# Optimization experiments

Hardware: AMD Instinct MI355X
Metric: run time of the kernel (lower is better)

## Reference

```python
import jax, jax.numpy as jnp
import numpy as np

N, SD, VD, ED, E, NG, NA, NB = 512, 256, 128, 128, 262144, 16, 16, 5


def _lin_init(key, fan_in, fan_out):
    # torch.nn.Linear default: U(-1/sqrt(fan_in), 1/sqrt(fan_in)); stored as (in, out)
    lim = 1.0 / np.sqrt(fan_in)
    return jax.random.uniform(key, (fan_in, fan_out), jnp.float32, -lim, lim)


def setup_inputs() -> dict:
    key = jax.random.key(0)
    ks = jax.random.split(key, 20)
    s = jax.random.normal(ks[0], (N, SD), jnp.float32)
    v = jax.random.normal(ks[1], (N, 3, VD), jnp.float32)
    p = jax.random.normal(ks[2], (N, 3), jnp.float32)
    e = jax.random.normal(ks[3], (E, ED), jnp.float32)
    batch = jnp.sort(jax.random.randint(ks[4], (N,), 0, NG))
    edge_index_global = jax.random.randint(ks[5], (2, E), 0, N)
    W_sm = _lin_init(ks[6], SD, SD); b_sm = jnp.zeros((SD,), jnp.float32)
    W_bm = _lin_init(ks[7], ED, SD); b_bm = jnp.zeros((SD,), jnp.float32)
    W_b0 = _lin_init(ks[8], SD + 1, SD); b_b0 = jnp.zeros((SD,), jnp.float32)
    W_b1 = _lin_init(ks[9], SD, NB); b_b1 = jnp.zeros((NB,), jnp.float32)
    W_c = _lin_init(ks[10], VD, 1)  # no bias
    W_a = _lin_init(ks[11], SD, NA); b_a = jnp.zeros((NA,), jnp.float32)
    return {"s": s, "v": v, "p": p, "e": e, "batch": batch,
            "edge_index_global": edge_index_global,
            "W_sm": W_sm, "b_sm": b_sm, "W_bm": W_bm, "b_bm": b_bm,
            "W_b0": W_b0, "b_b0": b_b0, "W_b1": W_b1, "b_b1": b_b1,
            "W_c": W_c, "W_a": W_a, "b_a": b_a}


def reference(s, v, p, e, batch, edge_index_global,
              W_sm, b_sm, W_bm, b_bm, W_b0, b_b0, W_b1, b_b1, W_c, W_a, b_a):
    # shared_mapping: Linear + SiLU
    s = jax.nn.silu(s @ W_sm + b_sm)                      # [N, SD]
    coords_pred = (v @ W_c)[..., 0]                       # [N, 3]
    atoms_pred = s @ W_a + b_a                            # [N, NA]
    j, i = edge_index_global[0], edge_index_global[1]
    n = s.shape[0]
    # coords_param == 'data': coords = p + pred, then per-graph mean centering
    coords_pred = p + coords_pred
    seg_sum = jax.ops.segment_sum(coords_pred, batch, num_segments=NG)
    counts = jax.ops.segment_sum(jnp.ones((n, 1), coords_pred.dtype), batch, num_segments=NG)
    mean = seg_sum / jnp.maximum(counts, 1.0)
    coords_pred = coords_pred - mean[batch]
    # squared pairwise distance per edge
    d = jnp.sum((coords_pred[i] - coords_pred[j]) ** 2, axis=-1, keepdims=True)  # [E, 1]
    # sparse -> dense -> sparse symmetrization of edge features (as in the source)
    e_dense = jnp.zeros((n, n, e.shape[-1]), e.dtype).at[j, i].set(e)
    e_dense = 0.5 * (e_dense + jnp.transpose(e_dense, (1, 0, 2)))
    e_sym = e_dense[j, i]                                 # [E, ED]
    f = s[i] + s[j] + (e_sym @ W_bm + b_bm)               # [E, SD]
    edge = jnp.concatenate([f, d], axis=-1)               # [E, SD+1]
    bonds_pred = jax.nn.silu(edge @ W_b0 + b_b0) @ W_b1 + b_b1  # [E, NB]
    return coords_pred, atoms_pred, bonds_pred
```

## Files before the change

### kernel.cpp

```cpp
#include <hip/hip_runtime.h>
#include <math.h>

#define N_NODES 512
#define SD_ 256
#define VD_ 128
#define ED_ 128
#define NE_ 262144
#define NG_ 16
#define NA_ 16
#define NB_ 5
#define MAXP 131328

typedef __attribute__((ext_vector_type(8))) short bf16x8;
typedef __attribute__((ext_vector_type(4))) float f32x4;

__device__ __forceinline__ float silu_f(float x) { return x / (1.0f + expf(-x)); }
__device__ __forceinline__ float silu_fast(float x) {
    return x * __builtin_amdgcn_rcpf(1.0f + __builtin_amdgcn_exp2f(x * -1.44269504f));
}
__device__ __forceinline__ unsigned short f2bf(float x) {
    unsigned int u = __float_as_uint(x);
    return (unsigned short)((u + 0x7fffu + ((u >> 16) & 1u)) >> 16);
}
__device__ __forceinline__ float bf2f(unsigned short h) {
    return __uint_as_float(((unsigned int)h) << 16);
}
__device__ __forceinline__ unsigned int cvt_pk_bf16(float lo, float hi) {
    unsigned int r;
    asm("v_cvt_pk_bf16_f32 %0, %1, %2" : "=v"(r) : "v"(lo), "v"(hi));
    return r;
}

__global__ __launch_bounds__(256) void prep_a(
    const int* __restrict__ ei, int* __restrict__ emap,
    const float* __restrict__ W_bm, const float* __restrict__ W_b0,
    unsigned short* __restrict__ WfF,
    const float* __restrict__ s, const float* __restrict__ v, const float* __restrict__ p,
    const float* __restrict__ W_sm, const float* __restrict__ b_sm,
    const float* __restrict__ W_a, const float* __restrict__ b_a,
    const float* __restrict__ W_c,
    const float* __restrict__ b_bm, const float* __restrict__ b_b0,
    float* __restrict__ s2f, float* __restrict__ cpred, float* __restrict__ atoms_out,
    int* __restrict__ counter, float* __restrict__ zrow, float* __restrict__ bias2)
{
    __shared__ float srow[8][SD_];
    __shared__ float s2row[8][SD_];
    const int bid = blockIdx.x;
    const int tid = threadIdx.x;

    if (bid < 1024) {
        int k = bid * 256 + tid;
        int j = ei[k], i = ei[NE_ + k];
        atomicMax(&emap[j * N_NODES + i], k);
        return;
    }
    if (bid < 1040) {
        int mtg = bid - 1024;
        int kb = tid >> 6;
        int l  = tid & 63;
        int m  = mtg * 16 + (l & 15);
        int k0 = kb * 32 + (l >> 4) * 8;
        float a8[8];
        #pragma unroll
        for (int i = 0; i < 8; ++i) a8[i] = 0.f;
        for (int c = 0; c < SD_; ++c) {
            float wb0 = W_b0[(size_t)c * SD_ + m];
            #pragma unroll
            for (int i = 0; i < 8; ++i)
                a8[i] = fmaf(W_bm[(size_t)(k0 + i) * SD_ + c], wb0, a8[i]);
        }
        bf16x8 pack;
        #pragma unroll
        for (int i = 0; i < 8; ++i) pack[i] = (short)f2bf(a8[i]);
        int idx = (mtg * 4 + kb) * 64 + l;
        *(bf16x8*)(WfF + (size_t)idx * 8) = pack;
        return;
    }
    if (bid < 1104) {
        const int n0 = (bid - 1040) * 8;
        #pragma unroll
        for (int n = 0; n < 8; ++n) srow[n][tid] = s[(size_t)(n0 + n) * SD_ + tid];
        __syncthreads();
        float acc[8];
        {
            float bb = b_sm[tid];
            #pragma unroll
            for (int n = 0; n < 8; ++n) acc[n] = bb;
        }
        #pragma unroll 4
        for (int c = 0; c < SD_; ++c) {
            float wv = W_sm[(size_t)c * SD_ + tid];
            #pragma unroll
            for (int n = 0; n < 8; ++n) acc[n] = fmaf(srow[n][c], wv, acc[n]);
        }
        #pragma unroll
        for (int n = 0; n < 8; ++n) {
            float sv = silu_f(acc[n]);
            s2f[(size_t)(n0 + n) * SD_ + tid] = sv;
            s2row[n][tid] = sv;
        }
        __syncthreads();
        if (tid < 128) {
            int n = tid >> 4, a = tid & 15;
            float x = b_a[a];
            #pragma unroll 8
            for (int c = 0; c < SD_; ++c) x = fmaf(s2row[n][c], W_a[(size_t)c * NA_ + a], x);
            atoms_out[(size_t)(n0 + n) * NA_ + a] = x;
        }
        return;
    }
    if (bid == 1104) {
        if (tid == 0) counter[0] = 0;
        if (tid < ED_) zrow[tid] = 0.0f;
        for (int o = tid; o < N_NODES * 3; o += 256) {
            float x = p[o];
            const float* vr = v + (size_t)o * VD_;
            #pragma unroll 8
            for (int c = 0; c < VD_; ++c) x = fmaf(vr[c], W_c[c], x);
            cpred[o] = x;
        }
        return;
    }
    {
        float acc = b_b0[tid];
        for (int c = 0; c < SD_; ++c)
            acc = fmaf(b_bm[c], W_b0[(size_t)c * SD_ + tid], acc);
        bias2[tid] = acc;
    }
}

__global__ __launch_bounds__(512) void prep_b(
    const float* __restrict__ cpred, const int* __restrict__ batch,
    float* __restrict__ coords_ws, float* __restrict__ coords_out,
    const int* __restrict__ emap, int* __restrict__ counter,
    int* __restrict__ pairslot, int4* __restrict__ worklist,
    const float* __restrict__ s2f, const float* __restrict__ W_b0,
    float* __restrict__ S2W)
{
    __shared__ float cl[N_NODES * 3];
    __shared__ int   bl[N_NODES];
    __shared__ float meanv[NG_ * 3];
    const int tid = threadIdx.x;
    const int bid = blockIdx.x;

    if (bid == 0) {
        bl[tid] = batch[tid];
        #pragma unroll
        for (int dd = 0; dd < 3; ++dd) cl[tid * 3 + dd] = cpred[tid * 3 + dd];
        __syncthreads();
        if (tid < NG_ * 3) {
            int g = tid / 3, dd = tid % 3;
            float sum = 0.f; int cnt = 0;
            for (int n = 0; n < N_NODES; ++n) {
                if (bl[n] == g) { sum += cl[n * 3 + dd]; cnt++; }
            }
            meanv[tid] = sum / (float)(cnt > 0 ? cnt : 1);
        }
        __syncthreads();
        int g = bl[tid];
        #pragma unroll
        for (int dd = 0; dd < 3; ++dd) {
            float val = cl[tid * 3 + dd] - meanv[g * 3 + dd];
            coords_ws[tid * 3 + dd]  = val;
            coords_out[tid * 3 + dd] = val;
        }
        return;
    }
    if (bid <= 512) {
        int idx = (bid - 1) * 512 + tid;
        int a = idx >> 9, b = idx & (N_NODES - 1);
        bool lower = (a <= b);
        int k1 = -1, k2 = -1;
        if (lower) {
            k1 = emap[(a << 9) | b];
            k2 = emap[(b << 9) | a];
        }
        bool qual = lower && (k1 >= 0 || k2 >= 0);
        unsigned long long mask = __ballot(qual);
        if (mask == 0ull) return;
        int lane = tid & 63;
        int leader = __ffsll((unsigned long long)mask) - 1;
        int base = 0;
        if (lane == leader) base = atomicAdd(counter, __popcll(mask));
        base = __shfl(base, leader);
        if (qual) {
            int slot = base + __popcll(mask & ((1ull << lane) - 1ull));
            pairslot[(a << 9) | b] = slot;
            pairslot[(b << 9) | a] = slot;
            worklist[slot] = make_int4(a, b, k1, k2);
        }
        return;
    }
    {
        __shared__ float srows[2][SD_];
        int n0 = (bid - 513) * 2;
        if (tid < 512) {
            int n = tid >> 8, c = tid & 255;
            srows[n][c] = s2f[(size_t)(n0 + n) * SD_ + c];
        }
        __syncthreads();
        int n = tid >> 8, m = tid & 255;
        float acc = 0.f;
        #pragma unroll 8
        for (int c = 0; c < SD_; ++c)
            acc = fmaf(srows[n][c], W_b0[(size_t)c * SD_ + m], acc);
        S2W[(size_t)(n0 + n) * SD_ + m] = acc;
    }
}

__global__ __launch_bounds__(256) void bonds_scatter(
    const int* __restrict__ ei, const int* __restrict__ pairslot,
    const float* __restrict__ repval, float* __restrict__ bonds_out)
{
    int k = blockIdx.x * 256 + threadIdx.x;
    int j = ei[k], i = ei[NE_ + k];
    int slot = pairslot[(j << 9) | i];
    const float* rp = repval + (size_t)slot * NB_;
    #pragma unroll
    for (int b = 0; b < NB_; ++b)
        bonds_out[(size_t)k * NB_ + b] = rp[b];
}

__global__ __launch_bounds__(512) void edge_mfma(
    const float* __restrict__ e, const int4* __restrict__ worklist,
    const int* __restrict__ counter, const float* __restrict__ coords,
    const float* __restrict__ zrow,
    const unsigned short* __restrict__ WfF, const float* __restrict__ S2W,
    const float* __restrict__ bias2,
    const float* __restrict__ W_b1, const float* __restrict__ W_b0_last,
    const float* __restrict__ b_b1,
    float* __restrict__ repval)
{
    const int blk = blockIdx.x;
    const int cnt = counter[0];
    if (blk * 64 >= cnt) return;

    __shared__ __align__(16) unsigned short esym_lds[64 * 128];
    __shared__ unsigned short wb1t[NB_ * 256];
    __shared__ float bonds_part[8 * 64 * NB_];
    __shared__ float dw[64];
    __shared__ int li_s[64], lj_s[64];

    const int tid = threadIdx.x;
    const int l   = tid & 63;
    const int w   = tid >> 6;
    const int eLo = l & 15;
    const int hi  = l >> 4;

    bf16x8 a1pf[4][2];
    #pragma unroll
    for (int kb = 0; kb < 4; ++kb)
        #pragma unroll
        for (int mt = 0; mt < 2; ++mt)
            a1pf[kb][mt] = *(const bf16x8*)(WfF + ((size_t)(((w * 2 + mt) * 4 + kb) * 64 + l) * 8));

    if (tid < 256) {
        const int eL = l;
        const int q  = w;
        int widx = min(blk * 64 + eL, cnt - 1);
        int4 wk = worklist[widx];
        const float* r1 = (wk.z >= 0) ? (e + (size_t)wk.z * ED_) : zrow;
        const float* r2 = (wk.w >= 0) ? (e + (size_t)wk.w * ED_) : zrow;
        const float4* p1 = (const float4*)(r1 + q * 32);
        const float4* p2 = (const float4*)(r2 + q * 32);
        float4 va[8], vb[8];
        #pragma unroll
        for (int t = 0; t < 8; ++t) va[t] = p1[t];
        #pragma unroll
        for (int t = 0; t < 8; ++t) vb[t] = p2[t];
        #pragma unroll
        for (int t = 0; t < 8; ++t) {
            va[t].x += vb[t].x; va[t].y += vb[t].y;
            va[t].z += vb[t].z; va[t].w += vb[t].w;
        }
        int ntB = eL >> 4, eLoB = eL & 15;
        #pragma unroll
        for (int h2 = 0; h2 < 4; ++h2) {
            float4 x0 = va[h2 * 2], x1 = va[h2 * 2 + 1];
            uint4 c;
            c.x = cvt_pk_bf16(0.5f * x0.x, 0.5f * x0.y);
            c.y = cvt_pk_bf16(0.5f * x0.z, 0.5f * x0.w);
            c.z = cvt_pk_bf16(0.5f * x1.x, 0.5f * x1.y);
            c.w = cvt_pk_bf16(0.5f * x1.z, 0.5f * x1.w);
            int chunk = (ntB * 4 + q) * 64 + h2 * 16 + eLoB;
            *(uint4*)(&esym_lds[chunk * 8]) = c;
        }
    } else {
        int t = tid - 256;
        #pragma unroll
        for (int b = 0; b < NB_; ++b)
            wb1t[b * 256 + t] = f2bf(W_b1[(size_t)t * NB_ + b]);
        if (t < 64) {
            int widx = min(blk * 64 + t, cnt - 1);
            int4 wk = worklist[widx];
            li_s[t] = wk.x; lj_s[t] = wk.y;
            float dx = coords[wk.x * 3 + 0] - coords[wk.y * 3 + 0];
            float dy = coords[wk.x * 3 + 1] - coords[wk.y * 3 + 1];
            float dz = coords[wk.x * 3 + 2] - coords[wk.y * 3 + 2];
            dw[t] = dx * dx + dy * dy + dz * dz;
        }
    }

    __syncthreads();

    f32x4 acc[2][4];
    #pragma unroll
    for (int mt = 0; mt < 2; ++mt) {
        int m0 = w * 32 + mt * 16 + hi * 4;
        float4 bz = *(const float4*)(bias2 + m0);
        float4 w2 = *(const float4*)(W_b0_last + m0);
        #pragma unroll
        for (int nt = 0; nt < 4; ++nt) {
            int pair = nt * 16 + eLo;
            int na = li_s[pair], nb2 = lj_s[pair];
            float4 sa  = *(const float4*)(S2W + (size_t)na  * SD_ + m0);
            float4 sb4 = *(const float4*)(S2W + (size_t)nb2 * SD_ + m0);
            float dd = dw[pair];
            acc[mt][nt] = (f32x4){fmaf(dd, w2.x, bz.x) + sa.x + sb4.x,
                                  fmaf(dd, w2.y, bz.y) + sa.y + sb4.y,
                                  fmaf(dd, w2.z, bz.z) + sa.z + sb4.z,
                                  fmaf(dd, w2.w, bz.w) + sa.w + sb4.w};
        }
    }

    #pragma unroll
    for (int kb = 0; kb < 4; ++kb) {
        bf16x8 bfg[4];
        #pragma unroll
        for (int nt = 0; nt < 4; ++nt)
            bfg[nt] = *(const bf16x8*)(&esym_lds[(size_t)((nt * 4 + kb) * 64 + l) * 8]);
        __builtin_amdgcn_s_setprio(1);
        #pragma unroll
        for (int mt = 0; mt < 2; ++mt)
            #pragma unroll
            for (int nt = 0; nt < 4; ++nt)
                acc[mt][nt] = __builtin_amdgcn_mfma_f32_16x16x32_bf16(a1pf[kb][mt], bfg[nt], acc[mt][nt], 0, 0, 0);
        __builtin_amdgcn_s_setprio(0);
    }

    float pb[4][NB_];
    #pragma unroll
    for (int nt = 0; nt < 4; ++nt)
        #pragma unroll
        for (int b = 0; b < NB_; ++b) pb[nt][b] = 0.f;
    #pragma unroll
    for (int mt = 0; mt < 2; ++mt) {
        int m0 = w * 32 + mt * 16 + hi * 4;
        ushort4 wv[NB_];
        #pragma unroll
        for (int b = 0; b < NB_; ++b)
            wv[b] = *(const ushort4*)(wb1t + b * 256 + m0);
        #pragma unroll
        for (int nt = 0; nt < 4; ++nt) {
            f32x4 r = acc[mt][nt];
            float h0 = silu_fast(r[0]);
            float h1 = silu_fast(r[1]);
            float h2 = silu_fast(r[2]);
            float h3 = silu_fast(r[3]);
            #pragma unroll
            for (int b = 0; b < NB_; ++b) {
                float t = fmaf(h0, bf2f(wv[b].x), fmaf(h1, bf2f(wv[b].y),
                          fmaf(h2, bf2f(wv[b].z), h3 * bf2f(wv[b].w))));
                pb[nt][b] += t;
            }
        }
    }
    #pragma unroll
    for (int off = 16; off <= 32; off <<= 1)
        #pragma unroll
        for (int nt = 0; nt < 4; ++nt)
            #pragma unroll
            for (int b = 0; b < NB_; ++b)
                pb[nt][b] += __shfl_xor(pb[nt][b], off);
    if (hi == 0) {
        #pragma unroll
        for (int nt = 0; nt < 4; ++nt)
            #pragma unroll
            for (int b = 0; b < NB_; ++b)
                bonds_part[(size_t)(w * 64 + nt * 16 + eLo) * NB_ + b] = pb[nt][b];
    }
    __syncthreads();

    for (int idx = tid; idx < 64 * NB_; idx += 512) {
        int edge = idx / NB_, b = idx % NB_;
        float s8 = 0.f;
        #pragma unroll
        for (int pp = 0; pp < 8; ++pp)
            s8 += bonds_part[(size_t)(pp * 64 + edge) * NB_ + b];
        repval[(size_t)(blk * 64 + edge) * NB_ + b] = s8 + b_b1[b];
    }
}

extern "C" void kernel_launch(void* const* d_in, const int* in_sizes, int n_in,
                              void* d_out, int out_size, void* d_ws, size_t ws_size,
                              hipStream_t stream)
{
    const float* s    = (const float*)d_in[0];
    const float* v    = (const float*)d_in[1];
    const float* p    = (const float*)d_in[2];
    const float* e    = (const float*)d_in[3];
    const int*   batch= (const int*)d_in[4];
    const int*   ei   = (const int*)d_in[5];
    const float* W_sm = (const float*)d_in[6];
    const float* b_sm = (const float*)d_in[7];
    const float* W_bm = (const float*)d_in[8];
    const float* b_bm = (const float*)d_in[9];
    const float* W_b0 = (const float*)d_in[10];
    const float* b_b0 = (const float*)d_in[11];
    const float* W_b1 = (const float*)d_in[12];
    const float* b_b1 = (const float*)d_in[13];
    const float* W_c  = (const float*)d_in[14];
    const float* W_a  = (const float*)d_in[15];
    const float* b_a  = (const float*)d_in[16];

    float* out = (float*)d_out;
    float* coords_out = out;
    float* atoms_out  = out + 1536;
    float* bonds_out  = out + 1536 + 8192;

    char* ws = (char*)d_ws;
    int*            emap    = (int*)ws;
    float*          s2f     = (float*)(ws + 0x100000);
    unsigned short* WfF     = (unsigned short*)(ws + 0x180000);
    float*          S2W     = (float*)(ws + 0x190000);
    float*          bias2   = (float*)(ws + 0x210000);
    float*          cpred   = (float*)(ws + 0x211000);
    float*          coords  = (float*)(ws + 0x213000);
    int*            counter = (int*)(ws + 0x215000);
    float*          zrow    = (float*)(ws + 0x215100);
    int*            pairslot= (int*)(ws + 0x2A0000);
    int4*           worklist= (int4*)(ws + 0x3A0000);
    float*          repval  = (float*)(ws + 0x5D0000);

    prep_a<<<1106, 256, 0, stream>>>(ei, emap, W_bm, W_b0, WfF,
                                     s, v, p, W_sm, b_sm, W_a, b_a, W_c,
                                     b_bm, b_b0,
                                     s2f, cpred, atoms_out, counter, zrow, bias2);
    prep_b<<<769, 512, 0, stream>>>(cpred, batch, coords, coords_out,
                                    emap, counter, pairslot, worklist,
                                    s2f, W_b0, S2W);

    edge_mfma<<<(MAXP + 63) / 64, 512, 0, stream>>>(e, worklist, counter, coords, zrow,
                                                    WfF, S2W, bias2,
                                                    W_b1, W_b0 + 256 * SD_, b_b1,
                                                    repval);
    bonds_scatter<<<NE_ / 256, 256, 0, stream>>>(ei, pairslot, repval, bonds_out);
}
```

Measured before the change: 130.2 us.

## Parallelize fused weight product across 128 blocks and defer half of A-fragment loads

The W_bm·W_b0 fused-weight precompute in prep_a moves from 16 blocks, each computing 8 outputs per thread with strided loads, to 128 blocks. Each new block stages one row of W_bm in LDS and computes a coalesced dot product per thread, and the block indices of the later roles shift to match. In edge_mfma only the first two k-blocks of A fragments are prefetched into registers and the remaining two are loaded from global inside the MFMA loop. This is meant to shorten the prep critical path and lower register pressure in the MFMA kernel, at the cost of extra global loads on the MFMA path.

Result: no change. 130.8 us (+0.5%).

```diff
diff --git a/kernel.cpp b/kernel.cpp
--- a/kernel.cpp
+++ b/kernel.cpp
@@ -54,30 +54,22 @@
         atomicMax(&emap[j * N_NODES + i], k);
         return;
     }
-    if (bid < 1040) {
-        int mtg = bid - 1024;
-        int kb = tid >> 6;
-        int l  = tid & 63;
-        int m  = mtg * 16 + (l & 15);
-        int k0 = kb * 32 + (l >> 4) * 8;
-        float a8[8];
-        #pragma unroll
-        for (int i = 0; i < 8; ++i) a8[i] = 0.f;
-        for (int c = 0; c < SD_; ++c) {
-            float wb0 = W_b0[(size_t)c * SD_ + m];
-            #pragma unroll
-            for (int i = 0; i < 8; ++i)
-                a8[i] = fmaf(W_bm[(size_t)(k0 + i) * SD_ + c], wb0, a8[i]);
-        }
-        bf16x8 pack;
-        #pragma unroll
-        for (int i = 0; i < 8; ++i) pack[i] = (short)f2bf(a8[i]);
-        int idx = (mtg * 4 + kb) * 64 + l;
-        *(bf16x8*)(WfF + (size_t)idx * 8) = pack;
-        return;
-    }
-    if (bid < 1104) {
-        const int n0 = (bid - 1040) * 8;
+    if (bid < 1152) {
+        int k = bid - 1024;
+        srow[0][tid] = W_bm[(size_t)k * SD_ + tid];
+        __syncthreads();
+        float acc = 0.f;
+        #pragma unroll 8
+        for (int c = 0; c < SD_; ++c)
+            acc = fmaf(srow[0][c], W_b0[(size_t)c * SD_ + tid], acc);
+        int mtg = tid >> 4, lo = tid & 15;
+        int kb = k >> 5, r = k & 31;
+        int l = ((r >> 3) << 4) | lo;
+        WfF[((size_t)((mtg * 4 + kb) * 64 + l) << 3) + (r & 7)] = f2bf(acc);
+        return;
+    }
+    if (bid < 1216) {
+        const int n0 = (bid - 1152) * 8;
         #pragma unroll
         for (int n = 0; n < 8; ++n) srow[n][tid] = s[(size_t)(n0 + n) * SD_ + tid];
         __syncthreads();
@@ -109,7 +101,7 @@
         }
         return;
     }
-    if (bid == 1104) {
+    if (bid == 1216) {
         if (tid == 0) counter[0] = 0;
         if (tid < ED_) zrow[tid] = 0.0f;
         for (int o = tid; o < N_NODES * 3; o += 256) {
@@ -247,9 +239,9 @@
     const int eLo = l & 15;
     const int hi  = l >> 4;
 
-    bf16x8 a1pf[4][2];
-    #pragma unroll
-    for (int kb = 0; kb < 4; ++kb)
+    bf16x8 a1pf[2][2];
+    #pragma unroll
+    for (int kb = 0; kb < 2; ++kb)
         #pragma unroll
         for (int mt = 0; mt < 2; ++mt)
             a1pf[kb][mt] = *(const bf16x8*)(WfF + ((size_t)(((w * 2 + mt) * 4 + kb) * 64 + l) * 8));
@@ -325,7 +317,11 @@
 
     #pragma unroll
     for (int kb = 0; kb < 4; ++kb) {
-        bf16x8 bfg[4];
+        bf16x8 af[2], bfg[4];
+        #pragma unroll
+        for (int mt = 0; mt < 2; ++mt)
+            af[mt] = (kb < 2) ? a1pf[kb][mt]
+                   : *(const bf16x8*)(WfF + ((size_t)(((w * 2 + mt) * 4 + kb) * 64 + l) * 8));
         #pragma unroll
         for (int nt = 0; nt < 4; ++nt)
             bfg[nt] = *(const bf16x8*)(&esym_lds[(size_t)((nt * 4 + kb) * 64 + l) * 8]);
@@ -334,7 +330,7 @@
         for (int mt = 0; mt < 2; ++mt)
             #pragma unroll
             for (int nt = 0; nt < 4; ++nt)
-                acc[mt][nt] = __builtin_amdgcn_mfma_f32_16x16x32_bf16(a1pf[kb][mt], bfg[nt], acc[mt][nt], 0, 0, 0);
+                acc[mt][nt] = __builtin_amdgcn_mfma_f32_16x16x32_bf16(af[mt], bfg[nt], acc[mt][nt], 0, 0, 0);
         __builtin_amdgcn_s_setprio(0);
     }
 
@@ -432,7 +428,7 @@
     int4*           worklist= (int4*)(ws + 0x3A0000);
     float*          repval  = (float*)(ws + 0x5D0000);
 
-    prep_a<<<1106, 256, 0, stream>>>(ei, emap, W_bm, W_b0, WfF,
+    prep_a<<<1218, 256, 0, stream>>>(ei, emap, W_bm, W_b0, WfF,
                                      s, v, p, W_sm, b_sm, W_a, b_a, W_c,
                                      b_bm, b_b0,
                                      s2f, cpred, atoms_out, counter, zrow, bias2);
```
